# Kernel tuning notes

Hardware: AMD Instinct MI355X
Metric: run time of the kernel (lower is better)

The kernel has to match this reference:

```python
import jax, jax.numpy as jnp
import numpy as np

D_MODEL = 1024
H = 16
D_K = D_MODEL // H


def setup_inputs() -> dict:
    key = jax.random.key(0)
    ks = jax.random.split(key, 13)
    B, S = 4, 2048
    scale = 1.0 / np.sqrt(D_MODEL)
    inp = {
        "query": jax.random.normal(ks[0], (B, S, D_MODEL), jnp.float32),
        "key": jax.random.normal(ks[1], (B, S, D_MODEL), jnp.float32),
        "value": jax.random.normal(ks[2], (B, S, D_MODEL), jnp.float32),
        "mask": jax.random.randint(ks[3], (B, S, S), 0, 2, jnp.int32),
        "Wq": jax.random.normal(ks[4], (D_MODEL, D_MODEL), jnp.float32) * scale,
        "bq": jnp.zeros((D_MODEL,), jnp.float32),
        "Wk": jax.random.normal(ks[5], (D_MODEL, D_MODEL), jnp.float32) * scale,
        "bk": jnp.zeros((D_MODEL,), jnp.float32),
        "Wv": jax.random.normal(ks[6], (D_MODEL, D_MODEL), jnp.float32) * scale,
        "bv": jnp.zeros((D_MODEL,), jnp.float32),
        "Wo": jax.random.normal(ks[7], (D_MODEL, D_MODEL), jnp.float32) * scale,
        "bo": jnp.zeros((D_MODEL,), jnp.float32),
    }
    return inp


def _split_heads(x):
    # [B, S, D] -> [B, H, S, d_k]
    B, S, _ = x.shape
    return x.reshape(B, S, H, D_K).transpose(0, 2, 1, 3)


def reference(query, key, value, mask, Wq, bq, Wk, bk, Wv, bv, Wo, bo):
    B, S, _ = query.shape
    q = _split_heads(query @ Wq + bq)
    k = _split_heads(key @ Wk + bk)
    v = _split_heads(value @ Wv + bv)
    # scores: [B, H, S, S]
    scores = jnp.einsum("bhqd,bhkd->bhqk", q, k) / jnp.sqrt(jnp.float32(D_K))
    scores = jnp.where(mask[:, None, :, :] == 0, jnp.float32(-1e9), scores)
    prob = jax.nn.softmax(scores, axis=-1)
    out = jnp.einsum("bhqk,bhkd->bhqd", prob, v)
    out = out.transpose(0, 2, 1, 3).reshape(B, S, D_MODEL)
    return out @ Wo + bo
```

## Files before the change

### kernel.cpp

```cpp
#include <hip/hip_runtime.h>
#include <hip/hip_bf16.h>


typedef __bf16 bf16;
typedef __bf16 bf16x4 __attribute__((ext_vector_type(4)));
typedef __bf16 bf16x8 __attribute__((ext_vector_type(8)));
typedef float f32x4 __attribute__((ext_vector_type(4)));
typedef float f32x16 __attribute__((ext_vector_type(16)));
typedef unsigned int uint;

__device__ __forceinline__ void gload_lds16(const void* g, void* l) {
  __builtin_amdgcn_global_load_lds(
      (__attribute__((address_space(1))) void*)g,
      (__attribute__((address_space(3))) void*)l, 16, 0, 0);
}

__global__ __launch_bounds__(256) void wt_kernel(const float* __restrict__ Wq,
                                                 const float* __restrict__ Wk,
                                                 const float* __restrict__ Wv,
                                                 const float* __restrict__ Wo,
                                                 bf16* __restrict__ wt) {
  __shared__ float tile[64][65];
  const int z = blockIdx.z;
  const float* W = (z == 0) ? Wq : (z == 1) ? Wk : (z == 2) ? Wv : Wo;
  bf16* out = wt + (size_t)z * 1048576;
  const int k0 = blockIdx.x * 64, n0 = blockIdx.y * 64;
  for (int e = threadIdx.x; e < 4096; e += 256) {
    int r = e >> 6, c = e & 63;
    tile[r][c] = W[(size_t)(k0 + r) * 1024 + n0 + c];
  }
  __syncthreads();
  for (int e = threadIdx.x; e < 4096; e += 256) {
    int r = e >> 6, c = e & 63;
    out[(size_t)(n0 + r) * 1024 + k0 + c] = (bf16)tile[c][r];
  }
}

__global__ __launch_bounds__(256) void maskpack_kernel(const int* __restrict__ mask,
                                                       unsigned long long* __restrict__ bits) {
  const int gid = blockIdx.x * 256 + threadIdx.x;
  const int word = gid >> 6;
  const int lane = threadIdx.x & 63;
  int v = mask[(size_t)word * 64 + lane];
  unsigned long long b = __ballot(v != 0);
  if (lane == 0) bits[word] = b;
}

template <int MODE>
__global__ __launch_bounds__(256) void gemm_kernel(const void* __restrict__ Aptr,
                                                   const bf16* __restrict__ Bt,
                                                   const float* __restrict__ bias,
                                                   void* __restrict__ Out) {
  __shared__ alignas(16) char smem[32768];
  char* As = smem;
  char* Bs = smem + 16384;
  const int t = threadIdx.x;
  const int w = t >> 6, l = t & 63;
  const int hi = l >> 4, lo = l & 15, l7 = l & 7;
  const int wr = w >> 1, wc = w & 1;
  const int row0 = blockIdx.x * 128;
  const int n0 = blockIdx.y * 128;

  const f32x4 fz = {0.f, 0.f, 0.f, 0.f};
  f32x4 acc[4][4];
#pragma unroll
  for (int mi = 0; mi < 4; ++mi)
#pragma unroll
    for (int ni = 0; ni < 4; ++ni) acc[mi][ni] = fz;

  for (int kt = 0; kt < 16; ++kt) {
    if constexpr (MODE < 3) {
      const float* A = (const float*)Aptr;
#pragma unroll
      for (int i = 0; i < 8; ++i) {
        int qq = i * 256 + t;
        int r = qq >> 4, q = qq & 15;
        f32x4 f = *(const f32x4*)(A + (size_t)(row0 + r) * 1024 + kt * 64 + q * 4);
        bf16x4 h = {(bf16)f[0], (bf16)f[1], (bf16)f[2], (bf16)f[3]};
        *(bf16x4*)(As + r * 128 + ((q * 8) ^ ((r & 7) << 4))) = h;
      }
    } else {
      const char* A = (const char*)Aptr;
#pragma unroll
      for (int i = 0; i < 4; ++i) {
        int c = i * 256 + t;
        int r = c >> 3, s = c & 7;
        gload_lds16(A + (size_t)(row0 + r) * 2048 + kt * 128 + ((s ^ (r & 7)) * 16),
                    As + (i * 256 + w * 64) * 16);
      }
    }
    {
      const char* Bb = (const char*)Bt;
#pragma unroll
      for (int i = 0; i < 4; ++i) {
        int c = i * 256 + t;
        int r = c >> 3, s = c & 7;
        gload_lds16(Bb + (size_t)(n0 + r) * 2048 + kt * 128 + ((s ^ (r & 7)) * 16),
                    Bs + (i * 256 + w * 64) * 16);
      }
    }
    __syncthreads();
#pragma unroll
    for (int kk = 0; kk < 2; ++kk) {
      bf16x8 af[4], bfr[4];
#pragma unroll
      for (int mi = 0; mi < 4; ++mi)
        af[mi] = *(const bf16x8*)(As + (wr * 64 + mi * 16 + lo) * 128 +
                                  ((kk * 64 + hi * 16) ^ (l7 << 4)));
#pragma unroll
      for (int ni = 0; ni < 4; ++ni)
        bfr[ni] = *(const bf16x8*)(Bs + (wc * 64 + ni * 16 + lo) * 128 +
                                   ((kk * 64 + hi * 16) ^ (l7 << 4)));
#pragma unroll
      for (int mi = 0; mi < 4; ++mi)
#pragma unroll
        for (int ni = 0; ni < 4; ++ni)
          acc[mi][ni] =
              __builtin_amdgcn_mfma_f32_16x16x32_bf16(af[mi], bfr[ni], acc[mi][ni], 0, 0, 0);
    }
    __syncthreads();
  }

#pragma unroll
  for (int mi = 0; mi < 4; ++mi)
#pragma unroll
    for (int ni = 0; ni < 4; ++ni) {
      int gcol = n0 + wc * 64 + ni * 16 + lo;
      float bv = bias[gcol];
#pragma unroll
      for (int j = 0; j < 4; ++j) {
        int grow = row0 + wr * 64 + mi * 16 + hi * 4 + j;
        float v = acc[mi][ni][j] + bv;
        if constexpr (MODE == 0) v *= 0.18033688011112042f;
        if constexpr (MODE <= 1) {
          int b = grow >> 11, si = grow & 2047, h = gcol >> 6, d = gcol & 63;
          ((bf16*)Out)[((((size_t)b * 16 + h) * 2048 + si) << 6) + d] = (bf16)v;
        } else if constexpr (MODE == 2) {
          int b = grow >> 11, si = grow & 2047, h = gcol >> 6, d = gcol & 63;
          ((bf16*)Out)[((((size_t)b * 16 + h) * 64 + d) << 11) + si] = (bf16)v;
        } else {
          ((float*)Out)[(size_t)grow * 1024 + gcol] = v;
        }
      }
    }
}

__global__ __launch_bounds__(256) void attn_kernel(const char* __restrict__ qb,
                                                   const char* __restrict__ kb,
                                                   const char* __restrict__ vb,
                                                   const unsigned long long* __restrict__ mbits,
                                                   bf16* __restrict__ out) {
  __shared__ alignas(16) char smem[32768];
  const int t = threadIdx.x;
  const int w = t >> 6, l = t & 63;
  const int q31 = l & 31, hi = l >> 5;
  const int bh = blockIdx.x, b = bh >> 4, h = bh & 15;
  const int q0 = blockIdx.y * 128;
  const int qrow = q0 + w * 32 + q31;

  bf16x8 qf[4];
#pragma unroll
  for (int kc = 0; kc < 4; ++kc)
    qf[kc] = *(const bf16x8*)(qb + (size_t)(bh * 2048 + qrow) * 128 + kc * 32 + hi * 16);

  const f32x16 fz16 = {0.f, 0.f, 0.f, 0.f, 0.f, 0.f, 0.f, 0.f,
                       0.f, 0.f, 0.f, 0.f, 0.f, 0.f, 0.f, 0.f};
  f32x16 o[2];
  o[0] = fz16;
  o[1] = fz16;
  float mreg = -3e38f, ls = 0.f;
  const unsigned long long* mrow = mbits + (size_t)(b * 2048 + qrow) * 32;

  for (int kt2 = 0; kt2 < 16; ++kt2) {
#pragma unroll
    for (int i = 0; i < 4; ++i) {
      int c = i * 256 + t;
      int kr = c >> 3, ks = c & 7;
      gload_lds16(kb + (size_t)(bh * 2048 + kt2 * 128 + kr) * 128 + ((ks ^ (kr & 7)) * 16),
                  smem + (i * 256 + w * 64) * 16);
      int vr = c >> 4, vs = c & 15;
      gload_lds16(vb + (size_t)(bh * 64 + vr) * 4096 + kt2 * 256 + ((vs ^ (vr & 7)) * 16),
                  smem + 16384 + (i * 256 + w * 64) * 16);
    }
    __syncthreads();

#pragma unroll
    for (int h2 = 0; h2 < 2; ++h2) {
      const int kt = kt2 * 2 + h2;
      const unsigned long long mw = mrow[kt];

      f32x16 sc[2];
      sc[0] = fz16;
      sc[1] = fz16;
      __builtin_amdgcn_s_setprio(1);
#pragma unroll
      for (int kc = 0; kc < 4; ++kc) {
        bf16x8 kf0 = *(const bf16x8*)(smem + (h2 * 64 + q31) * 128 +
                                      (((kc * 2 + hi) ^ (q31 & 7)) * 16));
        bf16x8 kf1 = *(const bf16x8*)(smem + (h2 * 64 + 32 + q31) * 128 +
                                      (((kc * 2 + hi) ^ (q31 & 7)) * 16));
        sc[0] = __builtin_amdgcn_mfma_f32_32x32x16_bf16(kf0, qf[kc], sc[0], 0, 0, 0);
        sc[1] = __builtin_amdgcn_mfma_f32_32x32x16_bf16(kf1, qf[kc], sc[1], 0, 0, 0);
      }
      __builtin_amdgcn_s_setprio(0);

      float sv[2][16];
      float tm = -3e38f;
#pragma unroll
      for (int n = 0; n < 2; ++n) {
        uint m32 = (uint)(mw >> (n * 32 + 4 * hi));
#pragma unroll
        for (int r = 0; r < 16; ++r) {
          const int bi = (r & 3) + 8 * (r >> 2);
          float x = ((m32 >> bi) & 1u) ? sc[n][r] : -1e9f;
          sv[n][r] = x;
          tm = fmaxf(tm, x);
        }
      }
      tm = fmaxf(tm, __shfl_xor(tm, 32));

      if (!__all(tm - mreg <= 4.f)) {
        float mn = fmaxf(mreg, tm);
        float scal = __builtin_amdgcn_exp2f(mreg - mn);
        ls *= scal;
        o[0] *= scal;
        o[1] *= scal;
        mreg = mn;
      }

      uint wpk[2][8];
#pragma unroll
      for (int n = 0; n < 2; ++n)
#pragma unroll
        for (int r2 = 0; r2 < 8; ++r2) {
          float p0 = __builtin_amdgcn_exp2f(sv[n][2 * r2] - mreg);
          float p1 = __builtin_amdgcn_exp2f(sv[n][2 * r2 + 1] - mreg);
          ls += p0 + p1;
          uint pk;
          asm("v_cvt_pk_bf16_f32 %0, %1, %2" : "=v"(pk) : "v"(p0), "v"(p1));
          wpk[n][r2] = pk;
        }

      __builtin_amdgcn_s_setprio(1);
#pragma unroll
      for (int n = 0; n < 2; ++n)
#pragma unroll
        for (int c2 = 0; c2 < 2; ++c2) {
          uint a0 = wpk[n][4 * c2], b0 = wpk[n][4 * c2 + 2];
          uint a1 = wpk[n][4 * c2 + 1], b1 = wpk[n][4 * c2 + 3];
          asm("v_permlane32_swap_b32 %0, %1" : "+v"(a0), "+v"(b0));
          asm("v_permlane32_swap_b32 %0, %1" : "+v"(a1), "+v"(b1));
          union {
            uint u[4];
            bf16x8 v;
          } pf;
          pf.u[0] = a0;
          pf.u[1] = a1;
          pf.u[2] = b0;
          pf.u[3] = b1;
          const int c = n * 2 + c2;
          const int slot = (h2 * 8 + c * 2 + hi);
          bf16x8 vf0 = *(const bf16x8*)(smem + 16384 + q31 * 256 +
                                        ((slot ^ (q31 & 7)) * 16));
          bf16x8 vf1 = *(const bf16x8*)(smem + 16384 + (32 + q31) * 256 +
                                        ((slot ^ (q31 & 7)) * 16));
          o[0] = __builtin_amdgcn_mfma_f32_32x32x16_bf16(vf0, pf.v, o[0], 0, 0, 0);
          o[1] = __builtin_amdgcn_mfma_f32_32x32x16_bf16(vf1, pf.v, o[1], 0, 0, 0);
        }
      __builtin_amdgcn_s_setprio(0);
    }
    __syncthreads();
  }

  ls += __shfl_xor(ls, 32);
  float inv = 1.f / ls;
  size_t rbase = (size_t)((b << 11) + qrow) * 1024 + h * 64;
#pragma unroll
  for (int db = 0; db < 2; ++db)
#pragma unroll
    for (int g = 0; g < 4; ++g) {
      bf16x4 hv = {(bf16)(o[db][4 * g] * inv), (bf16)(o[db][4 * g + 1] * inv),
                   (bf16)(o[db][4 * g + 2] * inv), (bf16)(o[db][4 * g + 3] * inv)};
      *(bf16x4*)(out + rbase + db * 32 + 8 * g + 4 * hi) = hv;
    }
}

extern "C" void kernel_launch(void* const* d_in, const int* in_sizes, int n_in,
                              void* d_out, int out_size, void* d_ws, size_t ws_size,
                              hipStream_t stream) {
  const float* query = (const float*)d_in[0];
  const float* key_ = (const float*)d_in[1];
  const float* value = (const float*)d_in[2];
  const int* mask = (const int*)d_in[3];
  const float* Wq = (const float*)d_in[4];
  const float* bq = (const float*)d_in[5];
  const float* Wk = (const float*)d_in[6];
  const float* bk = (const float*)d_in[7];
  const float* Wv = (const float*)d_in[8];
  const float* bv = (const float*)d_in[9];
  const float* Wo = (const float*)d_in[10];
  const float* bo = (const float*)d_in[11];

  char* ws = (char*)d_ws;
  bf16* wt = (bf16*)ws;
  char* qbuf = ws + 8388608;
  char* kbuf = qbuf + 16777216;
  char* vbuf = kbuf + 16777216;
  char* abuf = vbuf + 16777216;
  unsigned long long* mbits = (unsigned long long*)(abuf + 16777216);

  wt_kernel<<<dim3(16, 16, 4), 256, 0, stream>>>(Wq, Wk, Wv, Wo, wt);
  maskpack_kernel<<<65536, 256, 0, stream>>>(mask, mbits);
  gemm_kernel<0><<<dim3(64, 8), 256, 0, stream>>>(query, wt, bq, qbuf);
  gemm_kernel<1><<<dim3(64, 8), 256, 0, stream>>>(key_, wt + 1048576, bk, kbuf);
  gemm_kernel<2><<<dim3(64, 8), 256, 0, stream>>>(value, wt + 2097152, bv, vbuf);
  attn_kernel<<<dim3(64, 16), 256, 0, stream>>>(qbuf, kbuf, vbuf, mbits, (bf16*)abuf);
  gemm_kernel<3><<<dim3(64, 8), 256, 0, stream>>>(abuf, wt + 3145728, bo, d_out);
}
```

Before: 296.1 us.

## Merge QKV projections into one launch and read K/V directly from global in attention

The three Q/K/V projection GEMMs are folded into a single launch using blockIdx.z, which gives a larger grid and removes two launches. The attention kernel no longer stages K and V tiles through LDS with barriers. Each wave loads its K and V fragments straight from global memory, relying on cache reuse, and launch bounds now request 4 blocks per CU. This removes the __syncthreads and LDS traffic but exposes global-load latency and repeats the same loads across the four waves of a block.

```diff
diff --git a/kernel.cpp b/kernel.cpp
--- a/kernel.cpp
+++ b/kernel.cpp
@@ -46,11 +46,11 @@
   if (lane == 0) bits[word] = b;
 }
 
-template <int MODE>
-__global__ __launch_bounds__(256) void gemm_kernel(const void* __restrict__ Aptr,
-                                                   const bf16* __restrict__ Bt,
-                                                   const float* __restrict__ bias,
-                                                   void* __restrict__ Out) {
+__global__ __launch_bounds__(256) void qkv_gemm_kernel(
+    const float* __restrict__ Aq, const float* __restrict__ Ak, const float* __restrict__ Av,
+    const bf16* __restrict__ wt, const float* __restrict__ bqp, const float* __restrict__ bkp,
+    const float* __restrict__ bvp, char* __restrict__ qbuf, char* __restrict__ kbuf,
+    char* __restrict__ vbuf) {
   __shared__ alignas(16) char smem[32768];
   char* As = smem;
   char* Bs = smem + 16384;
@@ -60,6 +60,11 @@
   const int wr = w >> 1, wc = w & 1;
   const int row0 = blockIdx.x * 128;
   const int n0 = blockIdx.y * 128;
+  const int z = blockIdx.z;
+  const float* A = (z == 0) ? Aq : (z == 1) ? Ak : Av;
+  const char* Bb = (const char*)(wt + (size_t)z * 1048576);
+  const float* bias = (z == 0) ? bqp : (z == 1) ? bkp : bvp;
+  char* ob = (z == 0) ? qbuf : (z == 1) ? kbuf : vbuf;
 
   const f32x4 fz = {0.f, 0.f, 0.f, 0.f};
   f32x4 acc[4][4];
@@ -69,35 +74,20 @@
     for (int ni = 0; ni < 4; ++ni) acc[mi][ni] = fz;
 
   for (int kt = 0; kt < 16; ++kt) {
-    if constexpr (MODE < 3) {
-      const float* A = (const float*)Aptr;
-#pragma unroll
-      for (int i = 0; i < 8; ++i) {
-        int qq = i * 256 + t;
-        int r = qq >> 4, q = qq & 15;
-        f32x4 f = *(const f32x4*)(A + (size_t)(row0 + r) * 1024 + kt * 64 + q * 4);
-        bf16x4 h = {(bf16)f[0], (bf16)f[1], (bf16)f[2], (bf16)f[3]};
-        *(bf16x4*)(As + r * 128 + ((q * 8) ^ ((r & 7) << 4))) = h;
-      }
-    } else {
-      const char* A = (const char*)Aptr;
-#pragma unroll
-      for (int i = 0; i < 4; ++i) {
-        int c = i * 256 + t;
-        int r = c >> 3, s = c & 7;
-        gload_lds16(A + (size_t)(row0 + r) * 2048 + kt * 128 + ((s ^ (r & 7)) * 16),
-                    As + (i * 256 + w * 64) * 16);
-      }
-    }
-    {
-      const char* Bb = (const char*)Bt;
-#pragma unroll
-      for (int i = 0; i < 4; ++i) {
-        int c = i * 256 + t;
-        int r = c >> 3, s = c & 7;
-        gload_lds16(Bb + (size_t)(n0 + r) * 2048 + kt * 128 + ((s ^ (r & 7)) * 16),
-                    Bs + (i * 256 + w * 64) * 16);
-      }
+#pragma unroll
+    for (int i = 0; i < 8; ++i) {
+      int qq = i * 256 + t;
+      int r = qq >> 4, q = qq & 15;
+      f32x4 f = *(const f32x4*)(A + (size_t)(row0 + r) * 1024 + kt * 64 + q * 4);
+      bf16x4 hq = {(bf16)f[0], (bf16)f[1], (bf16)f[2], (bf16)f[3]};
+      *(bf16x4*)(As + r * 128 + ((q * 8) ^ ((r & 7) << 4))) = hq;
+    }
+#pragma unroll
+    for (int i = 0; i < 4; ++i) {
+      int c = i * 256 + t;
+      int r = c >> 3, s = c & 7;
+      gload_lds16(Bb + (size_t)(n0 + r) * 2048 + kt * 128 + ((s ^ (r & 7)) * 16),
+                  Bs + (i * 256 + w * 64) * 16);
     }
     __syncthreads();
 #pragma unroll
@@ -121,6 +111,7 @@
     __syncthreads();
   }
 
+  const float scale = (z == 0) ? 0.18033688011112042f : 1.0f;
 #pragma unroll
   for (int mi = 0; mi < 4; ++mi)
 #pragma unroll
@@ -130,27 +121,89 @@
 #pragma unroll
       for (int j = 0; j < 4; ++j) {
         int grow = row0 + wr * 64 + mi * 16 + hi * 4 + j;
-        float v = acc[mi][ni][j] + bv;
-        if constexpr (MODE == 0) v *= 0.18033688011112042f;
-        if constexpr (MODE <= 1) {
-          int b = grow >> 11, si = grow & 2047, h = gcol >> 6, d = gcol & 63;
-          ((bf16*)Out)[((((size_t)b * 16 + h) * 2048 + si) << 6) + d] = (bf16)v;
-        } else if constexpr (MODE == 2) {
-          int b = grow >> 11, si = grow & 2047, h = gcol >> 6, d = gcol & 63;
-          ((bf16*)Out)[((((size_t)b * 16 + h) * 64 + d) << 11) + si] = (bf16)v;
+        float v = (acc[mi][ni][j] + bv) * scale;
+        int b = grow >> 11, si = grow & 2047, hh = gcol >> 6, d = gcol & 63;
+        if (z < 2) {
+          ((bf16*)ob)[((((size_t)b * 16 + hh) * 2048 + si) << 6) + d] = (bf16)v;
         } else {
-          ((float*)Out)[(size_t)grow * 1024 + gcol] = v;
+          ((bf16*)ob)[((((size_t)b * 16 + hh) * 64 + d) << 11) + si] = (bf16)v;
         }
       }
     }
 }
 
-__global__ __launch_bounds__(256) void attn_kernel(const char* __restrict__ qb,
-                                                   const char* __restrict__ kb,
-                                                   const char* __restrict__ vb,
-                                                   const unsigned long long* __restrict__ mbits,
-                                                   bf16* __restrict__ out) {
+__global__ __launch_bounds__(256) void gemm3_kernel(const char* __restrict__ Aptr,
+                                                    const bf16* __restrict__ Bt,
+                                                    const float* __restrict__ bias,
+                                                    float* __restrict__ Out) {
   __shared__ alignas(16) char smem[32768];
+  char* As = smem;
+  char* Bs = smem + 16384;
+  const int t = threadIdx.x;
+  const int w = t >> 6, l = t & 63;
+  const int hi = l >> 4, lo = l & 15, l7 = l & 7;
+  const int wr = w >> 1, wc = w & 1;
+  const int row0 = blockIdx.x * 128;
+  const int n0 = blockIdx.y * 128;
+
+  const f32x4 fz = {0.f, 0.f, 0.f, 0.f};
+  f32x4 acc[4][4];
+#pragma unroll
+  for (int mi = 0; mi < 4; ++mi)
+#pragma unroll
+    for (int ni = 0; ni < 4; ++ni) acc[mi][ni] = fz;
+
+  for (int kt = 0; kt < 16; ++kt) {
+#pragma unroll
+    for (int i = 0; i < 4; ++i) {
+      int c = i * 256 + t;
+      int r = c >> 3, s = c & 7;
+      gload_lds16(Aptr + (size_t)(row0 + r) * 2048 + kt * 128 + ((s ^ (r & 7)) * 16),
+                  As + (i * 256 + w * 64) * 16);
+      gload_lds16((const char*)Bt + (size_t)(n0 + r) * 2048 + kt * 128 + ((s ^ (r & 7)) * 16),
+                  Bs + (i * 256 + w * 64) * 16);
+    }
+    __syncthreads();
+#pragma unroll
+    for (int kk = 0; kk < 2; ++kk) {
+      bf16x8 af[4], bfr[4];
+#pragma unroll
+      for (int mi = 0; mi < 4; ++mi)
+        af[mi] = *(const bf16x8*)(As + (wr * 64 + mi * 16 + lo) * 128 +
+                                  ((kk * 64 + hi * 16) ^ (l7 << 4)));
+#pragma unroll
+      for (int ni = 0; ni < 4; ++ni)
+        bfr[ni] = *(const bf16x8*)(Bs + (wc * 64 + ni * 16 + lo) * 128 +
+                                   ((kk * 64 + hi * 16) ^ (l7 << 4)));
+#pragma unroll
+      for (int mi = 0; mi < 4; ++mi)
+#pragma unroll
+        for (int ni = 0; ni < 4; ++ni)
+          acc[mi][ni] =
+              __builtin_amdgcn_mfma_f32_16x16x32_bf16(af[mi], bfr[ni], acc[mi][ni], 0, 0, 0);
+    }
+    __syncthreads();
+  }
+
+#pragma unroll
+  for (int mi = 0; mi < 4; ++mi)
+#pragma unroll
+    for (int ni = 0; ni < 4; ++ni) {
+      int gcol = n0 + wc * 64 + ni * 16 + lo;
+      float bv = bias[gcol];
+#pragma unroll
+      for (int j = 0; j < 4; ++j) {
+        int grow = row0 + wr * 64 + mi * 16 + hi * 4 + j;
+        Out[(size_t)grow * 1024 + gcol] = acc[mi][ni][j] + bv;
+      }
+    }
+}
+
+__global__ __launch_bounds__(256, 4) void attn_kernel(const char* __restrict__ qb,
+                                                      const char* __restrict__ kb,
+                                                      const char* __restrict__ vb,
+                                                      const unsigned long long* __restrict__ mbits,
+                                                      bf16* __restrict__ out) {
   const int t = threadIdx.x;
   const int w = t >> 6, l = t & 63;
   const int q31 = l & 31, hi = l >> 5;
@@ -162,6 +215,9 @@
 #pragma unroll
   for (int kc = 0; kc < 4; ++kc)
     qf[kc] = *(const bf16x8*)(qb + (size_t)(bh * 2048 + qrow) * 128 + kc * 32 + hi * 16);
+
+  const char* kh = kb + (size_t)bh * 262144;
+  const char* vh = vb + (size_t)bh * 262144;
 
   const f32x16 fz16 = {0.f, 0.f, 0.f, 0.f, 0.f, 0.f, 0.f, 0.f,
                        0.f, 0.f, 0.f, 0.f, 0.f, 0.f, 0.f, 0.f};
@@ -171,105 +227,84 @@
   float mreg = -3e38f, ls = 0.f;
   const unsigned long long* mrow = mbits + (size_t)(b * 2048 + qrow) * 32;
 
-  for (int kt2 = 0; kt2 < 16; ++kt2) {
-#pragma unroll
-    for (int i = 0; i < 4; ++i) {
-      int c = i * 256 + t;
-      int kr = c >> 3, ks = c & 7;
-      gload_lds16(kb + (size_t)(bh * 2048 + kt2 * 128 + kr) * 128 + ((ks ^ (kr & 7)) * 16),
-                  smem + (i * 256 + w * 64) * 16);
-      int vr = c >> 4, vs = c & 15;
-      gload_lds16(vb + (size_t)(bh * 64 + vr) * 4096 + kt2 * 256 + ((vs ^ (vr & 7)) * 16),
-                  smem + 16384 + (i * 256 + w * 64) * 16);
-    }
-    __syncthreads();
-
-#pragma unroll
-    for (int h2 = 0; h2 < 2; ++h2) {
-      const int kt = kt2 * 2 + h2;
-      const unsigned long long mw = mrow[kt];
-
-      f32x16 sc[2];
-      sc[0] = fz16;
-      sc[1] = fz16;
-      __builtin_amdgcn_s_setprio(1);
-#pragma unroll
-      for (int kc = 0; kc < 4; ++kc) {
-        bf16x8 kf0 = *(const bf16x8*)(smem + (h2 * 64 + q31) * 128 +
-                                      (((kc * 2 + hi) ^ (q31 & 7)) * 16));
-        bf16x8 kf1 = *(const bf16x8*)(smem + (h2 * 64 + 32 + q31) * 128 +
-                                      (((kc * 2 + hi) ^ (q31 & 7)) * 16));
-        sc[0] = __builtin_amdgcn_mfma_f32_32x32x16_bf16(kf0, qf[kc], sc[0], 0, 0, 0);
-        sc[1] = __builtin_amdgcn_mfma_f32_32x32x16_bf16(kf1, qf[kc], sc[1], 0, 0, 0);
-      }
-      __builtin_amdgcn_s_setprio(0);
-
-      float sv[2][16];
-      float tm = -3e38f;
-#pragma unroll
-      for (int n = 0; n < 2; ++n) {
-        uint m32 = (uint)(mw >> (n * 32 + 4 * hi));
-#pragma unroll
-        for (int r = 0; r < 16; ++r) {
-          const int bi = (r & 3) + 8 * (r >> 2);
-          float x = ((m32 >> bi) & 1u) ? sc[n][r] : -1e9f;
-          sv[n][r] = x;
-          tm = fmaxf(tm, x);
-        }
-      }
-      tm = fmaxf(tm, __shfl_xor(tm, 32));
-
-      if (!__all(tm - mreg <= 4.f)) {
-        float mn = fmaxf(mreg, tm);
-        float scal = __builtin_amdgcn_exp2f(mreg - mn);
-        ls *= scal;
-        o[0] *= scal;
-        o[1] *= scal;
-        mreg = mn;
-      }
-
-      uint wpk[2][8];
-#pragma unroll
-      for (int n = 0; n < 2; ++n)
-#pragma unroll
-        for (int r2 = 0; r2 < 8; ++r2) {
-          float p0 = __builtin_amdgcn_exp2f(sv[n][2 * r2] - mreg);
-          float p1 = __builtin_amdgcn_exp2f(sv[n][2 * r2 + 1] - mreg);
-          ls += p0 + p1;
-          uint pk;
-          asm("v_cvt_pk_bf16_f32 %0, %1, %2" : "=v"(pk) : "v"(p0), "v"(p1));
-          wpk[n][r2] = pk;
-        }
-
-      __builtin_amdgcn_s_setprio(1);
-#pragma unroll
-      for (int n = 0; n < 2; ++n)
-#pragma unroll
-        for (int c2 = 0; c2 < 2; ++c2) {
-          uint a0 = wpk[n][4 * c2], b0 = wpk[n][4 * c2 + 2];
-          uint a1 = wpk[n][4 * c2 + 1], b1 = wpk[n][4 * c2 + 3];
-          asm("v_permlane32_swap_b32 %0, %1" : "+v"(a0), "+v"(b0));
-          asm("v_permlane32_swap_b32 %0, %1" : "+v"(a1), "+v"(b1));
-          union {
-            uint u[4];
-            bf16x8 v;
-          } pf;
-          pf.u[0] = a0;
-          pf.u[1] = a1;
-          pf.u[2] = b0;
-          pf.u[3] = b1;
-          const int c = n * 2 + c2;
-          const int slot = (h2 * 8 + c * 2 + hi);
-          bf16x8 vf0 = *(const bf16x8*)(smem + 16384 + q31 * 256 +
-                                        ((slot ^ (q31 & 7)) * 16));
-          bf16x8 vf1 = *(const bf16x8*)(smem + 16384 + (32 + q31) * 256 +
-                                        ((slot ^ (q31 & 7)) * 16));
-          o[0] = __builtin_amdgcn_mfma_f32_32x32x16_bf16(vf0, pf.v, o[0], 0, 0, 0);
-          o[1] = __builtin_amdgcn_mfma_f32_32x32x16_bf16(vf1, pf.v, o[1], 0, 0, 0);
-        }
-      __builtin_amdgcn_s_setprio(0);
-    }
-    __syncthreads();
+  for (int kt = 0; kt < 32; ++kt) {
+    const unsigned long long mw = mrow[kt];
+
+    f32x16 sc[2];
+    sc[0] = fz16;
+    sc[1] = fz16;
+    __builtin_amdgcn_s_setprio(1);
+#pragma unroll
+    for (int kc = 0; kc < 4; ++kc) {
+      bf16x8 kf0 = *(const bf16x8*)(kh + (size_t)(kt * 64 + q31) * 128 + kc * 32 + hi * 16);
+      bf16x8 kf1 = *(const bf16x8*)(kh + (size_t)(kt * 64 + 32 + q31) * 128 + kc * 32 + hi * 16);
+      sc[0] = __builtin_amdgcn_mfma_f32_32x32x16_bf16(kf0, qf[kc], sc[0], 0, 0, 0);
+      sc[1] = __builtin_amdgcn_mfma_f32_32x32x16_bf16(kf1, qf[kc], sc[1], 0, 0, 0);
+    }
+    __builtin_amdgcn_s_setprio(0);
+
+    float sv[2][16];
+    float tm = -3e38f;
+#pragma unroll
+    for (int n = 0; n < 2; ++n) {
+      uint m32 = (uint)(mw >> (n * 32 + 4 * hi));
+#pragma unroll
+      for (int r = 0; r < 16; ++r) {
+        const int bi = (r & 3) + 8 * (r >> 2);
+        float x = ((m32 >> bi) & 1u) ? sc[n][r] : -1e9f;
+        sv[n][r] = x;
+        tm = fmaxf(tm, x);
+      }
+    }
+    tm = fmaxf(tm, __shfl_xor(tm, 32));
+
+    if (!__all(tm - mreg <= 4.f)) {
+      float mn = fmaxf(mreg, tm);
+      float scal = __builtin_amdgcn_exp2f(mreg - mn);
+      ls *= scal;
+      o[0] *= scal;
+      o[1] *= scal;
+      mreg = mn;
+    }
+
+    uint wpk[2][8];
+#pragma unroll
+    for (int n = 0; n < 2; ++n)
+#pragma unroll
+      for (int r2 = 0; r2 < 8; ++r2) {
+        float p0 = __builtin_amdgcn_exp2f(sv[n][2 * r2] - mreg);
+        float p1 = __builtin_amdgcn_exp2f(sv[n][2 * r2 + 1] - mreg);
+        ls += p0 + p1;
+        uint pk;
+        asm("v_cvt_pk_bf16_f32 %0, %1, %2" : "=v"(pk) : "v"(p0), "v"(p1));
+        wpk[n][r2] = pk;
+      }
+
+    __builtin_amdgcn_s_setprio(1);
+#pragma unroll
+    for (int n = 0; n < 2; ++n)
+#pragma unroll
+      for (int c2 = 0; c2 < 2; ++c2) {
+        uint a0 = wpk[n][4 * c2], b0 = wpk[n][4 * c2 + 2];
+        uint a1 = wpk[n][4 * c2 + 1], b1 = wpk[n][4 * c2 + 3];
+        asm("v_permlane32_swap_b32 %0, %1" : "+v"(a0), "+v"(b0));
+        asm("v_permlane32_swap_b32 %0, %1" : "+v"(a1), "+v"(b1));
+        union {
+          uint u[4];
+          bf16x8 v;
+        } pf;
+        pf.u[0] = a0;
+        pf.u[1] = a1;
+        pf.u[2] = b0;
+        pf.u[3] = b1;
+        const int c = n * 2 + c2;
+        bf16x8 vf0 = *(const bf16x8*)(vh + (size_t)q31 * 4096 + kt * 128 + c * 32 + hi * 16);
+        bf16x8 vf1 =
+            *(const bf16x8*)(vh + (size_t)(32 + q31) * 4096 + kt * 128 + c * 32 + hi * 16);
+        o[0] = __builtin_amdgcn_mfma_f32_32x32x16_bf16(vf0, pf.v, o[0], 0, 0, 0);
+        o[1] = __builtin_amdgcn_mfma_f32_32x32x16_bf16(vf1, pf.v, o[1], 0, 0, 0);
+      }
+    __builtin_amdgcn_s_setprio(0);
   }
 
   ls += __shfl_xor(ls, 32);
@@ -311,9 +346,8 @@
 
   wt_kernel<<<dim3(16, 16, 4), 256, 0, stream>>>(Wq, Wk, Wv, Wo, wt);
   maskpack_kernel<<<65536, 256, 0, stream>>>(mask, mbits);
-  gemm_kernel<0><<<dim3(64, 8), 256, 0, stream>>>(query, wt, bq, qbuf);
-  gemm_kernel<1><<<dim3(64, 8), 256, 0, stream>>>(key_, wt + 1048576, bk, kbuf);
-  gemm_kernel<2><<<dim3(64, 8), 256, 0, stream>>>(value, wt + 2097152, bv, vbuf);
+  qkv_gemm_kernel<<<dim3(64, 8, 3), 256, 0, stream>>>(query, key_, value, wt, bq, bk, bv,
+                                                      qbuf, kbuf, vbuf);
   attn_kernel<<<dim3(64, 16), 256, 0, stream>>>(qbuf, kbuf, vbuf, mbits, (bf16*)abuf);
-  gemm_kernel<3><<<dim3(64, 8), 256, 0, stream>>>(abuf, wt + 3145728, bo, d_out);
-}
+  gemm3_kernel<<<dim3(64, 8), 256, 0, stream>>>(abuf, wt + 3145728, bo, (float*)d_out);
+}
```

New measurement: 429.1 us. +44.9%, slower.
